# Optimization experiments

Measured on AMD Instinct MI355X. Metric: run time of the kernel, lower is better.

Reference implementation:

```python
import jax, jax.numpy as jnp
import numpy as np

N = 50000      # nodes
E = 600000     # edges
F_IN = 128     # num_node_features
H = 128        # hidden_channels
C = 10         # num_classes
G = 512        # graphs in batch
EPS = 1e-5


def setup_inputs() -> dict:
    key = jax.random.key(0)
    ks = jax.random.split(key, 12)
    x = jax.random.normal(ks[0], (N, F_IN), dtype=jnp.float32)
    edge_index = jax.random.randint(ks[1], (2, E), 0, N, dtype=jnp.int32)
    batch = jnp.sort(jax.random.randint(ks[2], (N,), 0, G, dtype=jnp.int32))
    s_in = 1.0 / np.sqrt(F_IN)
    s_h = 1.0 / np.sqrt(H)
    W1 = jax.random.uniform(ks[3], (H, F_IN), jnp.float32, -s_in, s_in)
    b1 = jax.random.uniform(ks[4], (H,), jnp.float32, -s_in, s_in)
    W2 = jax.random.uniform(ks[5], (H, H), jnp.float32, -s_h, s_h)
    b2 = jax.random.uniform(ks[6], (H,), jnp.float32, -s_h, s_h)
    W3 = jax.random.uniform(ks[7], (H, H), jnp.float32, -s_h, s_h)
    b3 = jax.random.uniform(ks[8], (H,), jnp.float32, -s_h, s_h)
    Wlin = jax.random.uniform(ks[9], (C, H), jnp.float32, -s_h, s_h)
    blin = jax.random.uniform(ks[10], (C,), jnp.float32, -s_h, s_h)
    return {"x": x, "edge_index": edge_index, "batch": batch,
            "W1": W1, "b1": b1, "W2": W2, "b2": b2, "W3": W3, "b3": b3,
            "Wlin": Wlin, "blin": blin}


def _gcn_norm(edge_index, num_nodes):
    # PyG GCNConv default: add self-loops, symmetric D^-1/2 A D^-1/2 norm
    loop = jnp.arange(num_nodes, dtype=edge_index.dtype)
    src = jnp.concatenate([edge_index[0], loop])
    dst = jnp.concatenate([edge_index[1], loop])
    deg = jax.ops.segment_sum(jnp.ones_like(dst, dtype=jnp.float32), dst,
                              num_segments=num_nodes)
    dinv = jnp.where(deg > 0, jax.lax.rsqrt(deg), 0.0)
    norm = dinv[src] * dinv[dst]  # [E+N]
    return src, dst, norm


def _gcn_conv(x, W, b, src, dst, norm, num_nodes):
    h = x @ W.T                                  # [N, H]
    msg = norm[:, None] * h[src]                 # gather: [E+N, H]
    out = jax.ops.segment_sum(msg, dst, num_segments=num_nodes)  # scatter-add
    return out + b


def _batchnorm(x):
    # BatchNorm1d(affine=False), training mode: batch stats, biased variance
    mu = jnp.mean(x, axis=0)
    var = jnp.mean(jnp.square(x - mu), axis=0)
    return (x - mu) * jax.lax.rsqrt(var + EPS)


def reference(x, edge_index, batch, W1, b1, W2, b2, W3, b3, Wlin, blin):
    src, dst, norm = _gcn_norm(edge_index, N)
    h = _gcn_conv(x, W1, b1, src, dst, norm, N)
    h = jax.nn.relu(_batchnorm(h))
    h = _gcn_conv(h, W2, b2, src, dst, norm, N)
    h = jax.nn.relu(_batchnorm(h))
    h = _gcn_conv(h, W3, b3, src, dst, norm, N)
    # global mean pool over graphs
    sums = jax.ops.segment_sum(h, batch, num_segments=G)
    cnts = jax.ops.segment_sum(jnp.ones((N,), jnp.float32), batch, num_segments=G)
    pooled = sums / jnp.maximum(cnts, 1.0)[:, None]   # [G, H]
    return pooled @ Wlin.T + blin                     # [G, C]
```

## Files before the change

kernel.cpp:

```cpp
#include <hip/hip_runtime.h>
#include <hip/hip_bf16.h>

#define NN 50000
#define NE 600000
#define FD 128
#define NG 512
#define NC 10
static constexpr float EPS_BN = 1e-5f;

typedef __bf16 bf16x8 __attribute__((ext_vector_type(8)));
typedef float f32x4 __attribute__((ext_vector_type(4)));

__device__ __forceinline__ unsigned short f2bf(float x) {
  unsigned u = __float_as_uint(x);
  u = (u + 0x7FFFu + ((u >> 16) & 1u)) >> 16;
  return (unsigned short)u;
}
__device__ __forceinline__ float bf2f(unsigned short h) {
  return __uint_as_float(((unsigned)h) << 16);
}

__global__ __launch_bounds__(256) void k_zero(float4* __restrict__ p) {
  int i = blockIdx.x * 256 + threadIdx.x;
  if (i < 13536) p[i] = make_float4(0.f, 0.f, 0.f, 0.f);
}

__global__ __launch_bounds__(256) void k_deg_scatter(const int* __restrict__ dst, float* __restrict__ deg) {
  int e = blockIdx.x * 256 + threadIdx.x;
  if (e < NE) unsafeAtomicAdd(&deg[dst[e]], 1.0f);
}

#define NB 196
__global__ __launch_bounds__(256) void k_bsum(const float* __restrict__ deg, int* __restrict__ bsum) {
  __shared__ int s[256];
  int t = threadIdx.x, i = blockIdx.x * 256 + t;
  s[t] = (i < NN) ? (int)deg[i] : 0;
  __syncthreads();
  for (int o = 128; o > 0; o >>= 1) { if (t < o) s[t] += s[t + o]; __syncthreads(); }
  if (t == 0) bsum[blockIdx.x] = s[0];
}

__global__ __launch_bounds__(256) void k_bscan(const int* __restrict__ bsum, int* __restrict__ bbase) {
  __shared__ int s[256];
  int t = threadIdx.x;
  int v = (t < NB) ? bsum[t] : 0;
  s[t] = v; __syncthreads();
  for (int o = 1; o < 256; o <<= 1) {
    int a = (t >= o) ? s[t - o] : 0; __syncthreads();
    s[t] += a; __syncthreads();
  }
  if (t < NB) bbase[t] = s[t] - v;
}

__global__ __launch_bounds__(256) void k_rowoff(float* __restrict__ deg, const int* __restrict__ bbase,
                                                int* __restrict__ row_off, int* __restrict__ cursor) {
  __shared__ int s[256];
  int t = threadIdx.x, i = blockIdx.x * 256 + t;
  float dv = (i < NN) ? deg[i] : 0.f;
  int c = (int)dv;
  s[t] = c; __syncthreads();
  for (int o = 1; o < 256; o <<= 1) {
    int a = (t >= o) ? s[t - o] : 0; __syncthreads();
    s[t] += a; __syncthreads();
  }
  int excl = s[t] - c + bbase[blockIdx.x];
  if (i <= NN) {
    row_off[i] = excl;
    if (i < NN) {
      cursor[i] = excl;
      deg[i] = rsqrtf(dv + 1.0f);
    }
  }
}

#define FILL_CHUNKS 293
#define PRE_FILL (8 * FILL_CHUNKS)
#define PRE_CVT  48
#define DRANGE 6250
__global__ __launch_bounds__(256) void k_pre(const int* __restrict__ src, const int* __restrict__ dst,
                                             const float* __restrict__ dinv, int* __restrict__ cursor,
                                             int2* __restrict__ csr,
                                             const float* __restrict__ W1, const float* __restrict__ W2,
                                             const float* __restrict__ W3, unsigned short* __restrict__ w2,
                                             const int* __restrict__ batch, int* __restrict__ gstart) {
  int b = blockIdx.x, t = threadIdx.x;
  if (b < PRE_FILL) {
    int g = b & 7;
    int chunk = b >> 3;
    int dlo = g * DRANGE, dhi = dlo + DRANGE;
    int e0 = chunk * 2048;
#pragma unroll
    for (int i = 0; i < 8; ++i) {
      int e = e0 + i * 256 + t;
      if (e < NE) {
        int d = dst[e];
        if (d >= dlo && d < dhi) {
          int s = src[e];
          float nrm = dinv[s] * dinv[d];
          int pos = atomicAdd(&cursor[d], 1);
          csr[pos] = make_int2(s, __float_as_int(nrm));
        }
      }
    }
  } else if (b < PRE_FILL + PRE_CVT) {
    int bb = b - PRE_FILL;
    int m = bb >> 4;
    const float* W = (m == 0) ? W1 : ((m == 1) ? W2 : W3);
    int i = (bb & 15) * 256 + t;
    float4 v = ((const float4*)W)[i];
    ushort4 hv, lv;
    hv.x = f2bf(v.x); lv.x = f2bf(v.x - bf2f(hv.x));
    hv.y = f2bf(v.y); lv.y = f2bf(v.y - bf2f(hv.y));
    hv.z = f2bf(v.z); lv.z = f2bf(v.z - bf2f(hv.z));
    hv.w = f2bf(v.w); lv.w = f2bf(v.w - bf2f(hv.w));
    int e0 = i * 4, row = e0 >> 7, col = e0 & 127;
    int sc_ = ((col & 120) ^ ((row & 7) << 3)) | (col & 7);
    unsigned short* base = w2 + m * 32768 + row * FD + sc_;
    *(ushort4*)base = hv;
    *(ushort4*)(base + 16384) = lv;
  } else {
    int g = (b - PRE_FILL - PRE_CVT) * 256 + t;
    if (g > NG) return;
    int lo = 0, hi = NN;
    while (lo < hi) {
      int mid = (lo + hi) >> 1;
      if (batch[mid] < g) lo = mid + 1; else hi = mid;
    }
    gstart[g] = lo;
  }
}

template <int BN>
__global__ __launch_bounds__(256) void k_gemm(const float* __restrict__ in, const float* __restrict__ bn8,
                                              const unsigned short* __restrict__ wsrc,
                                              unsigned short* __restrict__ hb) {
  __shared__ unsigned short w_lds[2 * FD * FD];
  __shared__ float s_musc[2 * FD];
  int t = threadIdx.x;
  {
    const uint4* s4 = (const uint4*)wsrc;
    uint4* d4 = (uint4*)w_lds;
#pragma unroll
    for (int c = 0; c < 16; ++c) d4[c * 256 + t] = s4[c * 256 + t];
  }
  if constexpr (BN != 0) {
    if (t < FD) {
      float s = 0.f, q = 0.f;
#pragma unroll
      for (int c = 0; c < 8; ++c) { s += bn8[c * FD + t]; q += bn8[1024 + c * FD + t]; }
      float m = s * (1.0f / NN);
      float v = fmaxf(q * (1.0f / NN) - m * m, 0.f);
      s_musc[t] = m;
      s_musc[FD + t] = rsqrtf(v + EPS_BN);
    }
  }
  __syncthreads();

  int w = t >> 6, l = t & 63;
  int rt = blockIdx.x * 4 + w;
  if (rt >= NN / 16) return;
  int r = l & 15, g = l >> 4;
  int ko = g * 8;
  f32x4 acc[8];
#pragma unroll
  for (int ct = 0; ct < 8; ++ct) acc[ct] = (f32x4){0.f, 0.f, 0.f, 0.f};

#pragma unroll
  for (int kk = 0; kk < FD; kk += 32) {
    float a0[8];
    {
      const float* p0 = in + (size_t)(rt * 16 + r) * FD + kk + ko;
      float4 x0 = *(const float4*)p0;
      float4 x1 = *(const float4*)(p0 + 4);
      a0[0] = x0.x; a0[1] = x0.y; a0[2] = x0.z; a0[3] = x0.w;
      a0[4] = x1.x; a0[5] = x1.y; a0[6] = x1.z; a0[7] = x1.w;
    }
    if constexpr (BN != 0) {
      const float* mp = s_musc + kk + ko;
      float4 m0 = *(const float4*)mp, m1 = *(const float4*)(mp + 4);
      float4 s0 = *(const float4*)(mp + FD), s1 = *(const float4*)(mp + FD + 4);
      float mu[8] = {m0.x, m0.y, m0.z, m0.w, m1.x, m1.y, m1.z, m1.w};
      float sc[8] = {s0.x, s0.y, s0.z, s0.w, s1.x, s1.y, s1.z, s1.w};
#pragma unroll
      for (int i = 0; i < 8; ++i)
        a0[i] = fmaxf((a0[i] - mu[i]) * sc[i], 0.f);
    }
    bf16x8 ah, al;
#pragma unroll
    for (int i = 0; i < 8; ++i) {
      __bf16 h0 = (__bf16)a0[i];
      ah[i] = h0; al[i] = (__bf16)(a0[i] - (float)h0);
    }
#pragma unroll
    for (int ct = 0; ct < 8; ++ct) {
      int row = ct * 16 + r;
      int idx = row * FD + ((kk + ko) ^ ((r & 7) << 3));
      bf16x8 bh = *(const bf16x8*)(w_lds + idx);
      bf16x8 bl = *(const bf16x8*)(w_lds + FD * FD + idx);
      acc[ct] = __builtin_amdgcn_mfma_f32_16x16x32_bf16(ah, bh, acc[ct], 0, 0, 0);
      acc[ct] = __builtin_amdgcn_mfma_f32_16x16x32_bf16(ah, bl, acc[ct], 0, 0, 0);
      acc[ct] = __builtin_amdgcn_mfma_f32_16x16x32_bf16(al, bh, acc[ct], 0, 0, 0);
    }
  }
#pragma unroll
  for (int ct = 0; ct < 8; ++ct)
#pragma unroll
    for (int i = 0; i < 4; ++i)
      hb[(size_t)(rt * 16 + g * 4 + i) * FD + ct * 16 + r] = f2bf(acc[ct][i]);
}

template <int STATS>
__global__ __launch_bounds__(256) void k_agg(const unsigned short* __restrict__ hb,
                                             const float* __restrict__ dinv,
                                             const float* __restrict__ bias, const int* __restrict__ row_off,
                                             const int2* __restrict__ csr, float* __restrict__ out,
                                             float* __restrict__ bn8) {
  int t = threadIdx.x;
  int n = blockIdx.x * 16 + (t >> 4);
  int q = t & 15;
  const uint4* hb4 = (const uint4*)hb;
  float dv = dinv[n];
  float s2 = dv * dv;
  float4 acc0 = ((const float4*)bias)[q * 2];
  float4 acc1 = ((const float4*)bias)[q * 2 + 1];
  {
    uint4 pv = hb4[(size_t)n * 16 + q];
    acc0.x = fmaf(s2, __uint_as_float(pv.x << 16), acc0.x);
    acc0.y = fmaf(s2, __uint_as_float(pv.x & 0xffff0000u), acc0.y);
    acc0.z = fmaf(s2, __uint_as_float(pv.y << 16), acc0.z);
    acc0.w = fmaf(s2, __uint_as_float(pv.y & 0xffff0000u), acc0.w);
    acc1.x = fmaf(s2, __uint_as_float(pv.z << 16), acc1.x);
    acc1.y = fmaf(s2, __uint_as_float(pv.z & 0xffff0000u), acc1.y);
    acc1.z = fmaf(s2, __uint_as_float(pv.w << 16), acc1.z);
    acc1.w = fmaf(s2, __uint_as_float(pv.w & 0xffff0000u), acc1.w);
  }
  int lo = row_off[n], hi = row_off[n + 1];
  for (int j = lo; j < hi; ++j) {
    int2 e = csr[j];
    float w = __int_as_float(e.y);
    uint4 pv = hb4[(size_t)e.x * 16 + q];
    acc0.x = fmaf(w, __uint_as_float(pv.x << 16), acc0.x);
    acc0.y = fmaf(w, __uint_as_float(pv.x & 0xffff0000u), acc0.y);
    acc0.z = fmaf(w, __uint_as_float(pv.y << 16), acc0.z);
    acc0.w = fmaf(w, __uint_as_float(pv.y & 0xffff0000u), acc0.w);
    acc1.x = fmaf(w, __uint_as_float(pv.z << 16), acc1.x);
    acc1.y = fmaf(w, __uint_as_float(pv.z & 0xffff0000u), acc1.y);
    acc1.z = fmaf(w, __uint_as_float(pv.w << 16), acc1.z);
    acc1.w = fmaf(w, __uint_as_float(pv.w & 0xffff0000u), acc1.w);
  }
  ((float4*)out)[(size_t)n * 32 + q * 2] = acc0;
  ((float4*)out)[(size_t)n * 32 + q * 2 + 1] = acc1;

  if constexpr (STATS != 0) {
    __shared__ float red_s[16][FD + 4], red_q[16][FD + 4];
    int slot = t >> 4, f = q * 8;
    red_s[slot][f + 0] = acc0.x; red_s[slot][f + 1] = acc0.y;
    red_s[slot][f + 2] = acc0.z; red_s[slot][f + 3] = acc0.w;
    red_s[slot][f + 4] = acc1.x; red_s[slot][f + 5] = acc1.y;
    red_s[slot][f + 6] = acc1.z; red_s[slot][f + 7] = acc1.w;
    red_q[slot][f + 0] = acc0.x * acc0.x; red_q[slot][f + 1] = acc0.y * acc0.y;
    red_q[slot][f + 2] = acc0.z * acc0.z; red_q[slot][f + 3] = acc0.w * acc0.w;
    red_q[slot][f + 4] = acc1.x * acc1.x; red_q[slot][f + 5] = acc1.y * acc1.y;
    red_q[slot][f + 6] = acc1.z * acc1.z; red_q[slot][f + 7] = acc1.w * acc1.w;
    __syncthreads();
    if (t < FD) {
      float s = 0.f, qq = 0.f;
#pragma unroll
      for (int m = 0; m < 16; ++m) { s += red_s[m][t]; qq += red_q[m][t]; }
      int c = (blockIdx.x & 7) * FD + t;
      unsafeAtomicAdd(&bn8[c], s);
      unsafeAtomicAdd(&bn8[1024 + c], qq);
    }
  }
}

__global__ __launch_bounds__(512) void k_poolfinal(const float* __restrict__ h, const int* __restrict__ gstart,
                                                   const float* __restrict__ Wlin, const float* __restrict__ blin,
                                                   float* __restrict__ out) {
  __shared__ float ps[4][FD];
  __shared__ float pp[FD];
  int g = blockIdx.x, t = threadIdx.x;
  int part = t >> 7, f = t & 127;
  int lo = gstart[g], hi = gstart[g + 1];
  float s = 0.f;
  for (int n = lo + part; n < hi; n += 4) s += h[(size_t)n * FD + f];
  ps[part][f] = s;
  __syncthreads();
  if (t < FD) {
    float tot = ps[0][t] + ps[1][t] + ps[2][t] + ps[3][t];
    pp[t] = tot * (1.0f / fmaxf((float)(hi - lo), 1.0f));
  }
  __syncthreads();
  if (t < NC) {
    float a = blin[t];
    for (int k = 0; k < FD; ++k) a = fmaf(pp[k], Wlin[t * FD + k], a);
    out[g * NC + t] = a;
  }
}

extern "C" void kernel_launch(void* const* d_in, const int* in_sizes, int n_in,
                              void* d_out, int out_size, void* d_ws, size_t ws_size,
                              hipStream_t stream) {
  const float* x    = (const float*)d_in[0];
  const int*   ei   = (const int*)d_in[1];
  const int*   batch= (const int*)d_in[2];
  const float* W1   = (const float*)d_in[3];
  const float* b1   = (const float*)d_in[4];
  const float* W2   = (const float*)d_in[5];
  const float* b2   = (const float*)d_in[6];
  const float* W3   = (const float*)d_in[7];
  const float* b3   = (const float*)d_in[8];
  const float* Wlin = (const float*)d_in[9];
  const float* blin = (const float*)d_in[10];
  float* out = (float*)d_out;
  float* ws  = (float*)d_ws;

  const int* srcI = ei;
  const int* dstI = ei + NE;

  float* deg    = ws;
  float* bnA    = ws + 50048;
  float* bnB    = bnA + 2048;
  float* bufB   = bnB + 2048;
  int2*  csr    = (int2*)(bufB + NN * FD);
  int*   row_off= (int*)(csr + NE);
  int*   cursor = row_off + 50048;
  int*   gstart = cursor + 50048;
  int*   bsum   = gstart + 1024;
  int*   bbase  = bsum + 256;
  unsigned short* w2 = (unsigned short*)(bbase + 256);
  unsigned short* hb = w2 + 3 * 32768;

  dim3 B(256);
  const int gE    = (NE + 255) / 256;
  const int gGemm = (NN / 16 + 3) / 4;
  const int gAgg  = NN / 16;

  k_zero<<<53, B, 0, stream>>>((float4*)ws);

  k_deg_scatter<<<gE, B, 0, stream>>>(dstI, deg);
  k_bsum<<<NB, B, 0, stream>>>(deg, bsum);
  k_bscan<<<1, B, 0, stream>>>(bsum, bbase);
  k_rowoff<<<NB, B, 0, stream>>>(deg, bbase, row_off, cursor);
  k_pre<<<PRE_FILL + PRE_CVT + 3, B, 0, stream>>>(srcI, dstI, deg, cursor, csr,
                                                  W1, W2, W3, w2, batch, gstart);

  k_gemm<0><<<gGemm, B, 0, stream>>>(x, nullptr, w2, hb);
  k_agg<1><<<gAgg, B, 0, stream>>>(hb, deg, b1, row_off, csr, bufB, bnA);

  k_gemm<1><<<gGemm, B, 0, stream>>>(bufB, bnA, w2 + 32768, hb);
  k_agg<1><<<gAgg, B, 0, stream>>>(hb, deg, b2, row_off, csr, bufB, bnB);

  k_gemm<1><<<gGemm, B, 0, stream>>>(bufB, bnB, w2 + 65536, hb);
  k_agg<0><<<gAgg, B, 0, stream>>>(hb, deg, b3, row_off, csr, bufB, nullptr);

  k_poolfinal<<<NG, 512, 0, stream>>>(bufB, gstart, Wlin, blin, out);
}
```

Baseline: 246.1 us.

## Drop low-half weight split, partition degree scatter, split fill kernel

The GEMM now stores only a bf16 high part of each weight, so it loads half as much into LDS and issues two MFMAs per tile instead of three (activations keep their hi/lo split). The degree-count scatter is rewritten to use the same destination-range partitioned grid as the CSR fill, which gives each block's atomics more locality. The row-offset/prefix step is merged with the weight conversion and graph-start search into one kernel, and the CSR fill becomes its own launch. Dropping the weight low part lowers GEMM accuracy to roughly bf16 on the weights, in exchange for less LDS traffic and fewer MFMA instructions.

```diff
diff --git a/kernel.cpp b/kernel.cpp
--- a/kernel.cpp
+++ b/kernel.cpp
@@ -25,9 +25,23 @@
   if (i < 13536) p[i] = make_float4(0.f, 0.f, 0.f, 0.f);
 }
 
+#define FILL_CHUNKS 293
+#define GRID_E8 (8 * FILL_CHUNKS)
+#define DRANGE 6250
 __global__ __launch_bounds__(256) void k_deg_scatter(const int* __restrict__ dst, float* __restrict__ deg) {
-  int e = blockIdx.x * 256 + threadIdx.x;
-  if (e < NE) unsafeAtomicAdd(&deg[dst[e]], 1.0f);
+  int b = blockIdx.x, t = threadIdx.x;
+  int g = b & 7;
+  int chunk = b >> 3;
+  int dlo = g * DRANGE, dhi = dlo + DRANGE;
+  int e0 = chunk * 2048;
+#pragma unroll
+  for (int i = 0; i < 8; ++i) {
+    int e = e0 + i * 256 + t;
+    if (e < NE) {
+      int d = dst[e];
+      if (d >= dlo && d < dhi) unsafeAtomicAdd(&deg[d], 1.0f);
+    }
+  }
 }
 
 #define NB 196
@@ -52,74 +66,43 @@
   if (t < NB) bbase[t] = s[t] - v;
 }
 
-__global__ __launch_bounds__(256) void k_rowoff(float* __restrict__ deg, const int* __restrict__ bbase,
-                                                int* __restrict__ row_off, int* __restrict__ cursor) {
-  __shared__ int s[256];
-  int t = threadIdx.x, i = blockIdx.x * 256 + t;
-  float dv = (i < NN) ? deg[i] : 0.f;
-  int c = (int)dv;
-  s[t] = c; __syncthreads();
-  for (int o = 1; o < 256; o <<= 1) {
-    int a = (t >= o) ? s[t - o] : 0; __syncthreads();
-    s[t] += a; __syncthreads();
-  }
-  int excl = s[t] - c + bbase[blockIdx.x];
-  if (i <= NN) {
-    row_off[i] = excl;
-    if (i < NN) {
-      cursor[i] = excl;
-      deg[i] = rsqrtf(dv + 1.0f);
-    }
-  }
-}
-
-#define FILL_CHUNKS 293
-#define PRE_FILL (8 * FILL_CHUNKS)
-#define PRE_CVT  48
-#define DRANGE 6250
-__global__ __launch_bounds__(256) void k_pre(const int* __restrict__ src, const int* __restrict__ dst,
-                                             const float* __restrict__ dinv, int* __restrict__ cursor,
-                                             int2* __restrict__ csr,
-                                             const float* __restrict__ W1, const float* __restrict__ W2,
-                                             const float* __restrict__ W3, unsigned short* __restrict__ w2,
-                                             const int* __restrict__ batch, int* __restrict__ gstart) {
+__global__ __launch_bounds__(256) void k_rowoff_cvt(float* __restrict__ deg, const int* __restrict__ bbase,
+                                                    int* __restrict__ row_off, int* __restrict__ cursor,
+                                                    const float* __restrict__ W1, const float* __restrict__ W2,
+                                                    const float* __restrict__ W3, unsigned short* __restrict__ w2,
+                                                    const int* __restrict__ batch, int* __restrict__ gstart) {
   int b = blockIdx.x, t = threadIdx.x;
-  if (b < PRE_FILL) {
-    int g = b & 7;
-    int chunk = b >> 3;
-    int dlo = g * DRANGE, dhi = dlo + DRANGE;
-    int e0 = chunk * 2048;
-#pragma unroll
-    for (int i = 0; i < 8; ++i) {
-      int e = e0 + i * 256 + t;
-      if (e < NE) {
-        int d = dst[e];
-        if (d >= dlo && d < dhi) {
-          int s = src[e];
-          float nrm = dinv[s] * dinv[d];
-          int pos = atomicAdd(&cursor[d], 1);
-          csr[pos] = make_int2(s, __float_as_int(nrm));
-        }
+  if (b < NB) {
+    __shared__ int s[256];
+    int i = b * 256 + t;
+    float dv = (i < NN) ? deg[i] : 0.f;
+    int c = (int)dv;
+    s[t] = c; __syncthreads();
+    for (int o = 1; o < 256; o <<= 1) {
+      int a = (t >= o) ? s[t - o] : 0; __syncthreads();
+      s[t] += a; __syncthreads();
+    }
+    int excl = s[t] - c + bbase[b];
+    if (i <= NN) {
+      row_off[i] = excl;
+      if (i < NN) {
+        cursor[i] = excl;
+        deg[i] = rsqrtf(dv + 1.0f);
       }
     }
-  } else if (b < PRE_FILL + PRE_CVT) {
-    int bb = b - PRE_FILL;
+  } else if (b < NB + 48) {
+    int bb = b - NB;
     int m = bb >> 4;
     const float* W = (m == 0) ? W1 : ((m == 1) ? W2 : W3);
     int i = (bb & 15) * 256 + t;
     float4 v = ((const float4*)W)[i];
-    ushort4 hv, lv;
-    hv.x = f2bf(v.x); lv.x = f2bf(v.x - bf2f(hv.x));
-    hv.y = f2bf(v.y); lv.y = f2bf(v.y - bf2f(hv.y));
-    hv.z = f2bf(v.z); lv.z = f2bf(v.z - bf2f(hv.z));
-    hv.w = f2bf(v.w); lv.w = f2bf(v.w - bf2f(hv.w));
+    ushort4 hv;
+    hv.x = f2bf(v.x); hv.y = f2bf(v.y); hv.z = f2bf(v.z); hv.w = f2bf(v.w);
     int e0 = i * 4, row = e0 >> 7, col = e0 & 127;
     int sc_ = ((col & 120) ^ ((row & 7) << 3)) | (col & 7);
-    unsigned short* base = w2 + m * 32768 + row * FD + sc_;
-    *(ushort4*)base = hv;
-    *(ushort4*)(base + 16384) = lv;
+    *(ushort4*)(w2 + m * FD * FD + row * FD + sc_) = hv;
   } else {
-    int g = (b - PRE_FILL - PRE_CVT) * 256 + t;
+    int g = (b - NB - 48) * 256 + t;
     if (g > NG) return;
     int lo = 0, hi = NN;
     while (lo < hi) {
@@ -130,18 +113,41 @@
   }
 }
 
+__global__ __launch_bounds__(256) void k_fill(const int* __restrict__ src, const int* __restrict__ dst,
+                                              const float* __restrict__ dinv, int* __restrict__ cursor,
+                                              int2* __restrict__ csr) {
+  int b = blockIdx.x, t = threadIdx.x;
+  int g = b & 7;
+  int chunk = b >> 3;
+  int dlo = g * DRANGE, dhi = dlo + DRANGE;
+  int e0 = chunk * 2048;
+#pragma unroll
+  for (int i = 0; i < 8; ++i) {
+    int e = e0 + i * 256 + t;
+    if (e < NE) {
+      int d = dst[e];
+      if (d >= dlo && d < dhi) {
+        int s = src[e];
+        float nrm = dinv[s] * dinv[d];
+        int pos = atomicAdd(&cursor[d], 1);
+        csr[pos] = make_int2(s, __float_as_int(nrm));
+      }
+    }
+  }
+}
+
 template <int BN>
 __global__ __launch_bounds__(256) void k_gemm(const float* __restrict__ in, const float* __restrict__ bn8,
                                               const unsigned short* __restrict__ wsrc,
                                               unsigned short* __restrict__ hb) {
-  __shared__ unsigned short w_lds[2 * FD * FD];
+  __shared__ unsigned short w_lds[FD * FD];
   __shared__ float s_musc[2 * FD];
   int t = threadIdx.x;
   {
     const uint4* s4 = (const uint4*)wsrc;
     uint4* d4 = (uint4*)w_lds;
 #pragma unroll
-    for (int c = 0; c < 16; ++c) d4[c * 256 + t] = s4[c * 256 + t];
+    for (int c = 0; c < 8; ++c) d4[c * 256 + t] = s4[c * 256 + t];
   }
   if constexpr (BN != 0) {
     if (t < FD) {
@@ -196,9 +202,7 @@
       int row = ct * 16 + r;
       int idx = row * FD + ((kk + ko) ^ ((r & 7) << 3));
       bf16x8 bh = *(const bf16x8*)(w_lds + idx);
-      bf16x8 bl = *(const bf16x8*)(w_lds + FD * FD + idx);
       acc[ct] = __builtin_amdgcn_mfma_f32_16x16x32_bf16(ah, bh, acc[ct], 0, 0, 0);
-      acc[ct] = __builtin_amdgcn_mfma_f32_16x16x32_bf16(ah, bl, acc[ct], 0, 0, 0);
       acc[ct] = __builtin_amdgcn_mfma_f32_16x16x32_bf16(al, bh, acc[ct], 0, 0, 0);
     }
   }
@@ -329,29 +333,27 @@
   int*   bsum   = gstart + 1024;
   int*   bbase  = bsum + 256;
   unsigned short* w2 = (unsigned short*)(bbase + 256);
-  unsigned short* hb = w2 + 3 * 32768;
+  unsigned short* hb = w2 + 3 * FD * FD;
 
   dim3 B(256);
-  const int gE    = (NE + 255) / 256;
   const int gGemm = (NN / 16 + 3) / 4;
   const int gAgg  = NN / 16;
 
   k_zero<<<53, B, 0, stream>>>((float4*)ws);
-
-  k_deg_scatter<<<gE, B, 0, stream>>>(dstI, deg);
+  k_deg_scatter<<<GRID_E8, B, 0, stream>>>(dstI, deg);
   k_bsum<<<NB, B, 0, stream>>>(deg, bsum);
   k_bscan<<<1, B, 0, stream>>>(bsum, bbase);
-  k_rowoff<<<NB, B, 0, stream>>>(deg, bbase, row_off, cursor);
-  k_pre<<<PRE_FILL + PRE_CVT + 3, B, 0, stream>>>(srcI, dstI, deg, cursor, csr,
-                                                  W1, W2, W3, w2, batch, gstart);
+  k_rowoff_cvt<<<NB + 48 + 3, B, 0, stream>>>(deg, bbase, row_off, cursor,
+                                              W1, W2, W3, w2, batch, gstart);
+  k_fill<<<GRID_E8, B, 0, stream>>>(srcI, dstI, deg, cursor, csr);
 
   k_gemm<0><<<gGemm, B, 0, stream>>>(x, nullptr, w2, hb);
   k_agg<1><<<gAgg, B, 0, stream>>>(hb, deg, b1, row_off, csr, bufB, bnA);
 
-  k_gemm<1><<<gGemm, B, 0, stream>>>(bufB, bnA, w2 + 32768, hb);
+  k_gemm<1><<<gGemm, B, 0, stream>>>(bufB, bnA, w2 + FD * FD, hb);
   k_agg<1><<<gAgg, B, 0, stream>>>(hb, deg, b2, row_off, csr, bufB, bnB);
 
-  k_gemm<1><<<gGemm, B, 0, stream>>>(bufB, bnB, w2 + 65536, hb);
+  k_gemm<1><<<gGemm, B, 0, stream>>>(bufB, bnB, w2 + 2 * FD * FD, hb);
   k_agg<0><<<gAgg, B, 0, stream>>>(hb, deg, b3, row_off, csr, bufB, nullptr);
 
   k_poolfinal<<<NG, 512, 0, stream>>>(bufB, gstart, Wlin, blin, out);
```

New measurement: 241.8 us. About the same (-1.7%).
